# Kernel optimization log

Measured on AMD Instinct MI355X. Metric: run time of the kernel, lower is better.

## Reference

```python
import jax, jax.numpy as jnp
import numpy as np

N, E, H_DIM, HEADS = 20000, 640000, 128, 8
HD = H_DIM // HEADS  # head_dim = 16


def setup_inputs() -> dict:
    key = jax.random.key(0)
    ks = jax.random.split(key, 12)
    def xavier(k, shape):
        fan_in, fan_out = shape[0], shape[1]
        lim = jnp.sqrt(6.0 / (fan_in + fan_out))
        return jax.random.uniform(k, shape, jnp.float32, -lim, lim)
    return {
        "x": jax.random.normal(ks[0], (N, H_DIM), jnp.float32),
        "edge_index": jax.random.randint(ks[1], (2, E), 0, N, jnp.int64 if jax.config.x64_enabled else jnp.int32),
        "edge_attr": jax.random.normal(ks[2], (E, H_DIM), jnp.float32),
        "WQ": xavier(ks[3], (H_DIM, H_DIM)),
        "WK": xavier(ks[4], (H_DIM, H_DIM)),
        "WV": xavier(ks[5], (H_DIM, H_DIM)),
        "WE": xavier(ks[6], (H_DIM, H_DIM)),
        "Wout": xavier(ks[7], (H_DIM, H_DIM)),
        "bout": jnp.zeros((H_DIM,), jnp.float32),
        "gn_w": jnp.ones((H_DIM,), jnp.float32),
        "gn_b": jnp.zeros((H_DIM,), jnp.float32),
        "gn_ms": jnp.ones((H_DIM,), jnp.float32),
    }


def reference(x, edge_index, edge_attr, WQ, WK, WV, WE, Wout, bout, gn_w, gn_b, gn_ms):
    n = x.shape[0]
    src, dst = edge_index[0], edge_index[1]  # PyG: row=source j, col=target i

    q = (x @ WQ).reshape(n, HEADS, HD)
    k = (x @ WK).reshape(n, HEADS, HD)
    v = (x @ WV).reshape(n, HEADS, HD)
    e = (edge_attr @ WE).reshape(-1, HEADS, HD)

    # per-edge attention score [E, HEADS]
    score = jnp.sum(q[dst] * (k[src] + e), axis=-1) / jnp.sqrt(jnp.asarray(HD, x.dtype))

    # scatter-softmax over edges grouped by destination node
    seg_max = jax.ops.segment_max(score, dst, num_segments=n)  # [N, HEADS]
    seg_max = jnp.where(jnp.isfinite(seg_max), seg_max, 0.0)
    ex = jnp.exp(score - seg_max[dst])
    denom = jax.ops.segment_sum(ex, dst, num_segments=n)
    alpha = ex / (denom[dst] + 1e-16)  # [E, HEADS]

    # weighted scatter-add aggregation
    msg = alpha[..., None] * (v[src] + e)  # [E, HEADS, HD]
    out = jax.ops.segment_sum(msg, dst, num_segments=n).reshape(n, H_DIM)

    out = out @ Wout + bout
    h = out + x  # residual (DropPath is identity in eval)

    # GraphNorm with batch=None -> single-graph normalization
    mean = jnp.mean(h, axis=0)
    o = h - mean * gn_ms
    var = jnp.mean(o * o, axis=0)
    o = gn_w * o / jnp.sqrt(var + 1e-5) + gn_b

    return jax.nn.gelu(o, approximate=False)
```

## Files before the change

kernel.cpp:

```cpp
#include <hip/hip_runtime.h>

using u16 = unsigned short;
using u32 = unsigned int;
typedef float f32x4 __attribute__((ext_vector_type(4)));
typedef short s16x8 __attribute__((ext_vector_type(8)));
typedef u32   u32x2 __attribute__((ext_vector_type(2)));
typedef u32   u32x4 __attribute__((ext_vector_type(4)));

__device__ __forceinline__ u16 f2bf(float f) {
  u32 u = __float_as_uint(f);
  u += 0x7fffu + ((u >> 16) & 1u);
  return (u16)(u >> 16);
}
__device__ __forceinline__ float bf2f(u16 h) {
  return __uint_as_float(((u32)h) << 16);
}

__global__ void ROEN_Final_33526514713351_kernel() {}


__global__ void roen_zero(int* __restrict__ count, int N, float* __restrict__ dbg) {
  int i = blockIdx.x * 256 + threadIdx.x;
  if (i == 0) dbg[0] = 1000.0f;
  if (i < N) count[i] = 0;
}

__global__ void roen_hist(const int* __restrict__ ei, int E, int* __restrict__ count,
                          float* __restrict__ dbg) {
  int i = blockIdx.x * 256 + threadIdx.x;
  if (i == 0) dbg[1] = 1001.0f;
  if (i < E) atomicAdd(&count[ei[E + i]], 1);
}

__global__ __launch_bounds__(256) void roen_scan(const int* __restrict__ count, int N,
                                                 int* __restrict__ off, int* __restrict__ cursor,
                                                 float* __restrict__ dbg) {
  __shared__ int tsum[256];
  int tid = threadIdx.x;
  if (tid == 0) dbg[2] = 1002.0f;
  int chunk = (N + 255) / 256;
  int b = tid * chunk;
  int e = b + chunk; if (e > N) e = N; if (b > N) b = N;
  int s = 0;
  for (int i = b; i < e; ++i) s += count[i];
  tsum[tid] = s;
  __syncthreads();
  for (int d = 1; d < 256; d <<= 1) {
    int t = (tid >= d) ? tsum[tid - d] : 0;
    __syncthreads();
    tsum[tid] += t;
    __syncthreads();
  }
  int run = tsum[tid] - s;
  for (int i = b; i < e; ++i) {
    off[i] = run; cursor[i] = run;
    run += count[i];
  }
  if (tid == 255) off[N] = run;
}

__global__ void roen_scatter(const int* __restrict__ ei, int E, int* __restrict__ cursor,
                             int* __restrict__ inv, int* __restrict__ srcS,
                             int* __restrict__ dstS, float* __restrict__ dbg) {
  int i = blockIdx.x * 256 + threadIdx.x;
  if (i == 0) dbg[3] = 1003.0f;
  if (i < E) {
    int s = ei[i];
    int d = ei[E + i];
    int p = atomicAdd(&cursor[d], 1);
    inv[i] = p;
    srcS[p] = s;
    dstS[p] = d;
  }
}

__global__ void roen_prep_w(const float* __restrict__ W0, const float* __restrict__ W1,
                            const float* __restrict__ W2, const float* __restrict__ W3,
                            const float* __restrict__ W4, u16* __restrict__ Wt,
                            float* __restrict__ dbg) {
  int w = blockIdx.x;
  if (w == 0 && threadIdx.x == 0) dbg[4] = 1004.0f;
  const float* W = (w == 0) ? W0 : (w == 1) ? W1 : (w == 2) ? W2 : (w == 3) ? W3 : W4;
  for (int idx = threadIdx.x; idx < 16384; idx += 256) {
    int n = idx >> 7, k = idx & 127;
    Wt[w * 16384 + idx] = f2bf(W[k * 128 + n]);
  }
}

__global__ __launch_bounds__(256) void roen_gemm_qkv(const float* __restrict__ x,
                                                     const u16* __restrict__ Wt,
                                                     u16* __restrict__ qb, u16* __restrict__ kb,
                                                     u32* __restrict__ vb2, int M,
                                                     float* __restrict__ dbg) {
  __shared__ u16 As[64 * 128];
  const int tid = threadIdx.x;
  if (blockIdx.x == 0 && tid == 0) dbg[5] = 1005.0f;
  const long brow = (long)blockIdx.x * 64;

  {
    f32x4 tmp[8];
#pragma unroll
    for (int j = 0; j < 8; ++j) {
      int idx = j * 256 + tid;
      int row = idx >> 5;
      int c4 = (idx & 31) * 4;
      long grow = brow + row;
      f32x4 a = {0.f, 0.f, 0.f, 0.f};
      if (grow < M) a = *(const f32x4*)(x + grow * 128 + c4);
      tmp[j] = a;
    }
#pragma unroll
    for (int j = 0; j < 8; ++j) {
      int idx = j * 256 + tid;
      int row = idx >> 5;
      int c4 = (idx & 31) * 4;
      u32 lo = ((u32)f2bf(tmp[j][1]) << 16) | (u32)f2bf(tmp[j][0]);
      u32 hi = ((u32)f2bf(tmp[j][3]) << 16) | (u32)f2bf(tmp[j][2]);
      int byte = (row * 256 + c4 * 2) ^ ((row & 7) << 4);
      u32x2 val; val[0] = lo; val[1] = hi;
      *(u32x2*)((char*)As + byte) = val;
    }
  }
  __syncthreads();

  const int wave = tid >> 6, lane = tid & 63;
  const int wc = wave * 32;
  const int lr = lane & 15, lg = lane >> 4;

  s16x8 af[4][4];
#pragma unroll
  for (int ks = 0; ks < 4; ++ks) {
    int kb2 = (ks * 32 + lg * 8) * 2;
#pragma unroll
    for (int mt = 0; mt < 4; ++mt) {
      int row = mt * 16 + lr;
      int byte = (row * 256 + kb2) ^ ((row & 7) << 4);
      af[ks][mt] = *(const s16x8*)((const char*)As + byte);
    }
  }

  for (int w = 0; w < 3; ++w) {
    s16x8 bfr[4][2];
#pragma unroll
    for (int ks = 0; ks < 4; ++ks)
#pragma unroll
      for (int nt = 0; nt < 2; ++nt)
        bfr[ks][nt] = *(const s16x8*)(Wt + w * 16384 + (wc + nt * 16 + lr) * 128 + ks * 32 + lg * 8);

    f32x4 acc[4][2];
    for (int mt = 0; mt < 4; ++mt)
      for (int nt = 0; nt < 2; ++nt) acc[mt][nt] = {0.f, 0.f, 0.f, 0.f};

#pragma unroll
    for (int ks = 0; ks < 4; ++ks)
      for (int mt = 0; mt < 4; ++mt)
        for (int nt = 0; nt < 2; ++nt)
          acc[mt][nt] = __builtin_amdgcn_mfma_f32_16x16x32_bf16(af[ks][mt], bfr[ks][nt], acc[mt][nt], 0, 0, 0);

    if (w == 2) {
      for (int mt = 0; mt < 4; ++mt) {
        for (int r = 0; r < 4; ++r) {
          long row = brow + mt * 16 + lg * 4 + r;
          if (row < M) {
            u32 val = (u32)f2bf(acc[mt][0][r]) | ((u32)f2bf(acc[mt][1][r]) << 16);
            vb2[row * 64 + wave * 16 + lr] = val;
          }
        }
      }
    } else {
      u16* C = (w == 0) ? qb : kb;
      for (int mt = 0; mt < 4; ++mt) {
        for (int nt = 0; nt < 2; ++nt) {
          int col = wc + nt * 16 + lr;
          for (int r = 0; r < 4; ++r) {
            long row = brow + mt * 16 + lg * 4 + r;
            if (row < M) C[row * 128 + col] = f2bf(acc[mt][nt][r]);
          }
        }
      }
    }
  }
}

__global__ __launch_bounds__(256) void roen_gemm_e(const float* __restrict__ ea,
                                                   const u16* __restrict__ WtE,
                                                   const int* __restrict__ inv,
                                                   u32* __restrict__ eS2, int E,
                                                   float* __restrict__ dbg) {
  __shared__ u16 As[128 * 128];
  __shared__ int invv[128];
  const int tid = threadIdx.x;
  if (blockIdx.x == 0 && tid == 0) dbg[6] = 1006.0f;
  const long brow = (long)blockIdx.x * 128;

  if (tid < 128) {
    long pos = brow + tid;
    invv[tid] = (pos < E) ? inv[pos] : -1;
  }

  {
    f32x4 tmp[16];
#pragma unroll
    for (int j = 0; j < 16; ++j) {
      int idx = j * 256 + tid;
      int row = idx >> 5;
      int c4 = (idx & 31) * 4;
      long grow = brow + row;
      f32x4 a = {0.f, 0.f, 0.f, 0.f};
      if (grow < E) a = *(const f32x4*)(ea + grow * 128 + c4);
      tmp[j] = a;
    }
#pragma unroll
    for (int j = 0; j < 16; ++j) {
      int idx = j * 256 + tid;
      int row = idx >> 5;
      int c4 = (idx & 31) * 4;
      u32 lo = ((u32)f2bf(tmp[j][1]) << 16) | (u32)f2bf(tmp[j][0]);
      u32 hi = ((u32)f2bf(tmp[j][3]) << 16) | (u32)f2bf(tmp[j][2]);
      int byte = (row * 256 + c4 * 2) ^ ((row & 7) << 4);
      u32x2 val; val[0] = lo; val[1] = hi;
      *(u32x2*)((char*)As + byte) = val;
    }
  }

  const int wave = tid >> 6, lane = tid & 63;
  const int wc = wave * 32;
  const int lr = lane & 15, lg = lane >> 4;

  s16x8 bfr[4][2];
#pragma unroll
  for (int ks = 0; ks < 4; ++ks)
#pragma unroll
    for (int nt = 0; nt < 2; ++nt)
      bfr[ks][nt] = *(const s16x8*)(WtE + (wc + nt * 16 + lr) * 128 + ks * 32 + lg * 8);

  __syncthreads();

  f32x4 acc[8][2];
  for (int mt = 0; mt < 8; ++mt)
    for (int nt = 0; nt < 2; ++nt) acc[mt][nt] = {0.f, 0.f, 0.f, 0.f};

  for (int ks = 0; ks < 4; ++ks) {
    int kb2 = (ks * 32 + lg * 8) * 2;
    s16x8 af[8];
    for (int mt = 0; mt < 8; ++mt) {
      int row = mt * 16 + lr;
      int byte = (row * 256 + kb2) ^ ((row & 7) << 4);
      af[mt] = *(const s16x8*)((const char*)As + byte);
    }
    for (int mt = 0; mt < 8; ++mt)
      for (int nt = 0; nt < 2; ++nt)
        acc[mt][nt] = __builtin_amdgcn_mfma_f32_16x16x32_bf16(af[mt], bfr[ks][nt], acc[mt][nt], 0, 0, 0);
  }

  for (int mt = 0; mt < 8; ++mt) {
    for (int r = 0; r < 4; ++r) {
      int row = mt * 16 + lg * 4 + r;
      int op = invv[row];
      if (op >= 0) {
        u32 val = (u32)f2bf(acc[mt][0][r]) | ((u32)f2bf(acc[mt][1][r]) << 16);
        eS2[(long)op * 64 + wave * 16 + lr] = val;
      }
    }
  }
}

__global__ __launch_bounds__(256) void roen_score(const int* __restrict__ srcS,
                                                  const int* __restrict__ dstS,
                                                  const u16* __restrict__ qb,
                                                  const u16* __restrict__ kb,
                                                  const u32* __restrict__ eS2,
                                                  float* __restrict__ wS, int E,
                                                  float* __restrict__ dbg) {
  long gid = (long)blockIdx.x * 256 + threadIdx.x;
  if (gid == 0) dbg[9] = 1009.0f;
  long pos = gid >> 3;
  int h = (int)(gid & 7);
  if (pos >= E) return;
  int dst = dstS[pos], src = srcS[pos];
  const s16x8* qp = (const s16x8*)(qb + (long)dst * 128 + h * 16);
  const s16x8* kp = (const s16x8*)(kb + (long)src * 128 + h * 16);
  const u32x4* ep = (const u32x4*)(eS2 + (long)pos * 64 + (h >> 1) * 16);
  const int sh = (h & 1) * 16;
  float acc = 0.f;
#pragma unroll
  for (int c = 0; c < 2; ++c) {
    s16x8 qv = qp[c], kv = kp[c];
    u32x4 ea_ = ep[c * 2], eb_ = ep[c * 2 + 1];
#pragma unroll
    for (int j = 0; j < 4; ++j) {
      float e0 = bf2f((u16)(ea_[j] >> sh));
      float e1 = bf2f((u16)(eb_[j] >> sh));
      acc += bf2f((u16)qv[j]) * (bf2f((u16)kv[j]) + e0);
      acc += bf2f((u16)qv[j + 4]) * (bf2f((u16)kv[j + 4]) + e1);
    }
  }
  wS[pos * 8 + h] = __expf(fminf(acc * 0.25f, 80.f));
}

__global__ __launch_bounds__(256) void roen_node_agg(const int* __restrict__ off,
                                                     const int* __restrict__ srcS,
                                                     const u32* __restrict__ eS2,
                                                     const u32* __restrict__ vb2,
                                                     const float* __restrict__ wS,
                                                     float* __restrict__ outat, int N,
                                                     float* __restrict__ dbg) {
  int wave = threadIdx.x >> 6;
  int lane = threadIdx.x & 63;
  int node = blockIdx.x * 4 + wave;
  if (node == 0 && lane == 0) dbg[10] = 1010.0f;
  if (node >= N) return;
  int beg = off[node], end = off[node + 1];

  const int dA = 32 * (lane >> 4) + (lane & 15);
  const int dB = dA + 16;
  const int hA = dA >> 4;
  const int hB = hA + 1;
  float accA = 0.f, accB = 0.f, dsA = 0.f, dsB = 0.f;

  int pos = beg;
  for (; pos + 4 <= end; pos += 4) {
    int s0 = srcS[pos], s1 = srcS[pos + 1], s2 = srcS[pos + 2], s3 = srcS[pos + 3];
    float wa0 = wS[(long)(pos + 0) * 8 + hA], wb0 = wS[(long)(pos + 0) * 8 + hB];
    float wa1 = wS[(long)(pos + 1) * 8 + hA], wb1 = wS[(long)(pos + 1) * 8 + hB];
    float wa2 = wS[(long)(pos + 2) * 8 + hA], wb2 = wS[(long)(pos + 2) * 8 + hB];
    float wa3 = wS[(long)(pos + 3) * 8 + hA], wb3 = wS[(long)(pos + 3) * 8 + hB];
    u32 e0 = eS2[(long)(pos + 0) * 64 + lane];
    u32 e1 = eS2[(long)(pos + 1) * 64 + lane];
    u32 e2 = eS2[(long)(pos + 2) * 64 + lane];
    u32 e3 = eS2[(long)(pos + 3) * 64 + lane];
    u32 v0 = vb2[(long)s0 * 64 + lane];
    u32 v1 = vb2[(long)s1 * 64 + lane];
    u32 v2 = vb2[(long)s2 * 64 + lane];
    u32 v3 = vb2[(long)s3 * 64 + lane];
    accA += wa0 * (bf2f((u16)v0) + bf2f((u16)e0));
    accB += wb0 * (bf2f((u16)(v0 >> 16)) + bf2f((u16)(e0 >> 16)));
    accA += wa1 * (bf2f((u16)v1) + bf2f((u16)e1));
    accB += wb1 * (bf2f((u16)(v1 >> 16)) + bf2f((u16)(e1 >> 16)));
    accA += wa2 * (bf2f((u16)v2) + bf2f((u16)e2));
    accB += wb2 * (bf2f((u16)(v2 >> 16)) + bf2f((u16)(e2 >> 16)));
    accA += wa3 * (bf2f((u16)v3) + bf2f((u16)e3));
    accB += wb3 * (bf2f((u16)(v3 >> 16)) + bf2f((u16)(e3 >> 16)));
    dsA += wa0 + wa1 + wa2 + wa3;
    dsB += wb0 + wb1 + wb2 + wb3;
  }
  for (; pos < end; ++pos) {
    float wa = wS[(long)pos * 8 + hA], wb = wS[(long)pos * 8 + hB];
    u32 ev = eS2[(long)pos * 64 + lane];
    int src = srcS[pos];
    u32 vv = vb2[(long)src * 64 + lane];
    accA += wa * (bf2f((u16)vv) + bf2f((u16)ev));
    accB += wb * (bf2f((u16)(vv >> 16)) + bf2f((u16)(ev >> 16)));
    dsA += wa; dsB += wb;
  }
  outat[(long)node * 128 + dA] = accA / (dsA + 1e-16f);
  outat[(long)node * 128 + dB] = accB / (dsB + 1e-16f);
}

__global__ __launch_bounds__(256) void roen_gemm_out(const float* __restrict__ A,
                                                     const u16* __restrict__ Wt,
                                                     const float* __restrict__ x,
                                                     const float* __restrict__ bo,
                                                     float* __restrict__ h,
                                                     float* __restrict__ psum,
                                                     float* __restrict__ psumsq, int M,
                                                     float* __restrict__ dbg) {
  __shared__ u16 As[64 * 128];
  const int tid = threadIdx.x;
  if (blockIdx.x == 0 && tid == 0) dbg[11] = 1011.0f;
  const long brow = (long)blockIdx.x * 64;

  {
    f32x4 tmp[8];
#pragma unroll
    for (int j = 0; j < 8; ++j) {
      int idx = j * 256 + tid;
      int row = idx >> 5;
      int c4 = (idx & 31) * 4;
      long grow = brow + row;
      f32x4 a = {0.f, 0.f, 0.f, 0.f};
      if (grow < M) a = *(const f32x4*)(A + grow * 128 + c4);
      tmp[j] = a;
    }
#pragma unroll
    for (int j = 0; j < 8; ++j) {
      int idx = j * 256 + tid;
      int row = idx >> 5;
      int c4 = (idx & 31) * 4;
      u32 lo = ((u32)f2bf(tmp[j][1]) << 16) | (u32)f2bf(tmp[j][0]);
      u32 hi = ((u32)f2bf(tmp[j][3]) << 16) | (u32)f2bf(tmp[j][2]);
      int byte = (row * 256 + c4 * 2) ^ ((row & 7) << 4);
      u32x2 val; val[0] = lo; val[1] = hi;
      *(u32x2*)((char*)As + byte) = val;
    }
  }

  const int wave = tid >> 6, lane = tid & 63;
  const int wc = wave * 32;
  const int lr = lane & 15, lg = lane >> 4;

  s16x8 bfr[4][2];
#pragma unroll
  for (int ks = 0; ks < 4; ++ks)
#pragma unroll
    for (int nt = 0; nt < 2; ++nt)
      bfr[ks][nt] = *(const s16x8*)(Wt + (wc + nt * 16 + lr) * 128 + ks * 32 + lg * 8);

  __syncthreads();

  f32x4 acc[4][2];
  for (int mt = 0; mt < 4; ++mt)
    for (int nt = 0; nt < 2; ++nt) acc[mt][nt] = {0.f, 0.f, 0.f, 0.f};

  for (int ks = 0; ks < 4; ++ks) {
    int kb2 = (ks * 32 + lg * 8) * 2;
    s16x8 af[4];
    for (int mt = 0; mt < 4; ++mt) {
      int row = mt * 16 + lr;
      int byte = (row * 256 + kb2) ^ ((row & 7) << 4);
      af[mt] = *(const s16x8*)((const char*)As + byte);
    }
    for (int mt = 0; mt < 4; ++mt)
      for (int nt = 0; nt < 2; ++nt)
        acc[mt][nt] = __builtin_amdgcn_mfma_f32_16x16x32_bf16(af[mt], bfr[ks][nt], acc[mt][nt], 0, 0, 0);
  }

  float b0 = bo[wc + lr];
  float b1 = bo[wc + 16 + lr];
  float cs[2] = {0.f, 0.f}, cs2[2] = {0.f, 0.f};
  for (int mt = 0; mt < 4; ++mt) {
    for (int nt = 0; nt < 2; ++nt) {
      int col = wc + nt * 16 + lr;
      float bb = (nt == 0) ? b0 : b1;
      for (int r = 0; r < 4; ++r) {
        long row = brow + mt * 16 + lg * 4 + r;
        if (row < M) {
          long idx = row * 128 + col;
          float val = acc[mt][nt][r] + bb + x[idx];
          h[idx] = val;
          cs[nt] += val;
          cs2[nt] += val * val;
        }
      }
    }
  }
#pragma unroll
  for (int nt = 0; nt < 2; ++nt) {
    cs[nt] += __shfl_xor(cs[nt], 16);
    cs[nt] += __shfl_xor(cs[nt], 32);
    cs2[nt] += __shfl_xor(cs2[nt], 16);
    cs2[nt] += __shfl_xor(cs2[nt], 32);
  }
  if (lg == 0) {
    int col0 = wc + lr;
    psum[(long)blockIdx.x * 128 + col0] = cs[0];
    psumsq[(long)blockIdx.x * 128 + col0] = cs2[0];
    psum[(long)blockIdx.x * 128 + col0 + 16] = cs[1];
    psumsq[(long)blockIdx.x * 128 + col0 + 16] = cs2[1];
  }
}

__global__ void roen_stats(const float* __restrict__ psum, const float* __restrict__ psumsq,
                           const float* __restrict__ gnw, const float* __restrict__ gnb,
                           const float* __restrict__ gnms, float* __restrict__ Ac,
                           float* __restrict__ Bc, int nb, int N, float* __restrict__ dbg) {
  int d = threadIdx.x;
  if (d == 0) dbg[13] = 1013.0f;
  float s = 0.f, s2 = 0.f;
  for (int i = 0; i < nb; ++i) {
    s += psum[(long)i * 128 + d];
    s2 += psumsq[(long)i * 128 + d];
  }
  float mean = s / (float)N;
  float mm = mean * gnms[d];
  float var = s2 / (float)N - 2.f * mm * mean + mm * mm;
  float scale = gnw[d] * rsqrtf(var + 1e-5f);
  Ac[d] = scale;
  Bc[d] = gnb[d] - mm * scale;
}

__global__ __launch_bounds__(256) void roen_final(const float* __restrict__ h,
                                                  const float* __restrict__ Ac,
                                                  const float* __restrict__ Bc,
                                                  float* __restrict__ out, long total) {
  long i = (long)blockIdx.x * 256 + threadIdx.x;
  if (i >= total) return;
  int d = (int)(i & 127);
  float v = h[i] * Ac[d] + Bc[d];
  out[i] = 0.5f * v * (1.f + erff(v * 0.70710678f));
}

extern "C" void kernel_launch(void* const* d_in, const int* in_sizes, int n_in,
                              void* d_out, int out_size, void* d_ws, size_t ws_size,
                              hipStream_t stream) {
  const float* x   = (const float*)d_in[0];
  const int*   ei  = (const int*)d_in[1];
  const float* ea  = (const float*)d_in[2];
  const float* WQ  = (const float*)d_in[3];
  const float* WK  = (const float*)d_in[4];
  const float* WV  = (const float*)d_in[5];
  const float* WE  = (const float*)d_in[6];
  const float* Wo  = (const float*)d_in[7];
  const float* bo  = (const float*)d_in[8];
  const float* gnw = (const float*)d_in[9];
  const float* gnb = (const float*)d_in[10];
  const float* gnms= (const float*)d_in[11];
  float* out = (float*)d_out;
  float* dbg = (float*)d_out;

  const int N = in_sizes[0] / 128;
  const int E = in_sizes[1] / 2;
  const int gN = (N + 63) / 64;

  char* base = (char*)d_ws;
  size_t cur = 0;
  auto alloc = [&](size_t bytes) -> char* {
    char* r = base + cur;
    cur = (cur + bytes + 255) & ~(size_t)255;
    return r;
  };
  u16*   wt     = (u16*)alloc(5 * 16384 * sizeof(u16));
  u16*   qb     = (u16*)alloc((size_t)N * 128 * sizeof(u16));
  u16*   kb     = (u16*)alloc((size_t)N * 128 * sizeof(u16));
  u32*   vb2    = (u32*)alloc((size_t)N * 64 * sizeof(u32));
  float* wS     = (float*)alloc((size_t)E * 8 * sizeof(float));
  int*   count  = (int*)alloc((size_t)N * sizeof(int));
  int*   offar  = (int*)alloc((size_t)(N + 1) * sizeof(int));
  int*   cursor = (int*)alloc((size_t)N * sizeof(int));
  int*   invar  = (int*)alloc((size_t)E * sizeof(int));
  int*   srcS   = (int*)alloc((size_t)E * sizeof(int));
  int*   dstS   = (int*)alloc((size_t)E * sizeof(int));
  float* outat  = (float*)alloc((size_t)N * 128 * sizeof(float));
  float* psum   = (float*)alloc((size_t)gN * 128 * sizeof(float));
  float* psumsq = (float*)alloc((size_t)gN * 128 * sizeof(float));
  float* Ac     = (float*)alloc(128 * sizeof(float));
  float* Bc     = (float*)alloc(128 * sizeof(float));
  u32*   eS2    = (u32*)alloc((size_t)E * 64 * sizeof(u32));
  float* hbuf   = (float*)eS2;

  roen_zero<<<(N + 255) / 256, 256, 0, stream>>>(count, N, dbg);
  roen_hist<<<(E + 255) / 256, 256, 0, stream>>>(ei, E, count, dbg);
  roen_scan<<<1, 256, 0, stream>>>(count, N, offar, cursor, dbg);
  roen_scatter<<<(E + 255) / 256, 256, 0, stream>>>(ei, E, cursor, invar, srcS, dstS, dbg);
  roen_prep_w<<<5, 256, 0, stream>>>(WQ, WK, WV, WE, Wo, wt, dbg);

  roen_gemm_qkv<<<gN, 256, 0, stream>>>(x, wt, qb, kb, vb2, N, dbg);
  roen_gemm_e<<<(E + 127) / 128, 256, 0, stream>>>(ea, wt + 3 * 16384, invar, eS2, E, dbg);

  roen_score<<<(int)(((long)E * 8 + 255) / 256), 256, 0, stream>>>(srcS, dstS, qb, kb, eS2, wS, E, dbg);
  roen_node_agg<<<(N + 3) / 4, 256, 0, stream>>>(offar, srcS, eS2, vb2, wS, outat, N, dbg);

  roen_gemm_out<<<gN, 256, 0, stream>>>(outat, wt + 4 * 16384, x, bo, hbuf, psum, psumsq, N, dbg);
  roen_stats<<<1, 128, 0, stream>>>(psum, psumsq, gnw, gnb, gnms, Ac, Bc, gN, N, dbg);
  roen_final<<<(int)(((long)N * 128 + 255) / 256), 256, 0, stream>>>(hbuf, Ac, Bc, out, (long)N * 128);
}
```

Baseline: 457.6 us.

## Capture atomic ranks for CSR build, parallelize scan, shrink edge GEMM tiles

The histogram kernel now records each edge's atomic rank, so the scatter computes its position as off[d]+rank and no longer needs a second atomic pass over a cursor array. The single-block scan becomes a 1024-thread wave-shuffle scan in place of a 256-thread serial chunked scan. The edge GEMM tile drops from 128 to 64 rows per block, which halves LDS use so more blocks fit per CU. The node aggregation loads its two head weights with one 2-float vector load. The CSR order within each node now follows the histogram atomics, and an extra E-sized rank array is written and read.

Measured after the change: 415.3 us. -9.2%, faster.

```diff
diff --git a/kernel.cpp b/kernel.cpp
--- a/kernel.cpp
+++ b/kernel.cpp
@@ -3,6 +3,7 @@
 using u16 = unsigned short;
 using u32 = unsigned int;
 typedef float f32x4 __attribute__((ext_vector_type(4)));
+typedef float f32x2 __attribute__((ext_vector_type(2)));
 typedef short s16x8 __attribute__((ext_vector_type(8)));
 typedef u32   u32x2 __attribute__((ext_vector_type(2)));
 typedef u32   u32x4 __attribute__((ext_vector_type(4)));
@@ -26,50 +27,62 @@
 }
 
 __global__ void roen_hist(const int* __restrict__ ei, int E, int* __restrict__ count,
-                          float* __restrict__ dbg) {
+                          int* __restrict__ rank, float* __restrict__ dbg) {
   int i = blockIdx.x * 256 + threadIdx.x;
   if (i == 0) dbg[1] = 1001.0f;
-  if (i < E) atomicAdd(&count[ei[E + i]], 1);
-}
-
-__global__ __launch_bounds__(256) void roen_scan(const int* __restrict__ count, int N,
-                                                 int* __restrict__ off, int* __restrict__ cursor,
-                                                 float* __restrict__ dbg) {
-  __shared__ int tsum[256];
-  int tid = threadIdx.x;
-  if (tid == 0) dbg[2] = 1002.0f;
-  int chunk = (N + 255) / 256;
-  int b = tid * chunk;
-  int e = b + chunk; if (e > N) e = N; if (b > N) b = N;
-  int s = 0;
-  for (int i = b; i < e; ++i) s += count[i];
-  tsum[tid] = s;
+  if (i < E) rank[i] = atomicAdd(&count[ei[E + i]], 1);
+}
+
+__global__ __launch_bounds__(1024) void roen_scan(const int* __restrict__ count, int N,
+                                                  int* __restrict__ off,
+                                                  float* __restrict__ dbg) {
+  __shared__ int wsum[16];
+  __shared__ int carrys;
+  int tid = threadIdx.x, lane = tid & 63, wv = tid >> 6;
+  if (tid == 0) { dbg[2] = 1002.0f; carrys = 0; }
   __syncthreads();
-  for (int d = 1; d < 256; d <<= 1) {
-    int t = (tid >= d) ? tsum[tid - d] : 0;
+  for (int base = 0; base < N; base += 1024) {
+    int i = base + tid;
+    int v = (i < N) ? count[i] : 0;
+    int x = v;
+#pragma unroll
+    for (int s = 1; s < 64; s <<= 1) {
+      int t = __shfl_up(x, s);
+      if (lane >= s) x += t;
+    }
+    if (lane == 63) wsum[wv] = x;
     __syncthreads();
-    tsum[tid] += t;
+    if (wv == 0 && lane < 16) {
+      int y = wsum[lane];
+#pragma unroll
+      for (int s = 1; s < 16; s <<= 1) {
+        int t = __shfl_up(y, s);
+        if (lane >= s) y += t;
+      }
+      wsum[lane] = y;
+    }
     __syncthreads();
-  }
-  int run = tsum[tid] - s;
-  for (int i = b; i < e; ++i) {
-    off[i] = run; cursor[i] = run;
-    run += count[i];
-  }
-  if (tid == 255) off[N] = run;
-}
-
-__global__ void roen_scatter(const int* __restrict__ ei, int E, int* __restrict__ cursor,
+    int wbase = (wv == 0) ? 0 : wsum[wv - 1];
+    int incl = x + wbase + carrys;
+    if (i < N) off[i] = incl - v;
+    __syncthreads();
+    if (tid == 1023) carrys = incl;
+    __syncthreads();
+  }
+  if (tid == 0) off[N] = carrys;
+}
+
+__global__ void roen_scatter(const int* __restrict__ ei, const int* __restrict__ off,
+                             const int* __restrict__ rank, int E,
                              int* __restrict__ inv, int* __restrict__ srcS,
                              int* __restrict__ dstS, float* __restrict__ dbg) {
   int i = blockIdx.x * 256 + threadIdx.x;
   if (i == 0) dbg[3] = 1003.0f;
   if (i < E) {
-    int s = ei[i];
     int d = ei[E + i];
-    int p = atomicAdd(&cursor[d], 1);
+    int p = off[d] + rank[i];
     inv[i] = p;
-    srcS[p] = s;
+    srcS[p] = ei[i];
     dstS[p] = d;
   }
 }
@@ -187,21 +200,21 @@
                                                    const int* __restrict__ inv,
                                                    u32* __restrict__ eS2, int E,
                                                    float* __restrict__ dbg) {
-  __shared__ u16 As[128 * 128];
-  __shared__ int invv[128];
+  __shared__ u16 As[64 * 128];
+  __shared__ int invv[64];
   const int tid = threadIdx.x;
   if (blockIdx.x == 0 && tid == 0) dbg[6] = 1006.0f;
-  const long brow = (long)blockIdx.x * 128;
-
-  if (tid < 128) {
+  const long brow = (long)blockIdx.x * 64;
+
+  if (tid < 64) {
     long pos = brow + tid;
     invv[tid] = (pos < E) ? inv[pos] : -1;
   }
 
   {
-    f32x4 tmp[16];
-#pragma unroll
-    for (int j = 0; j < 16; ++j) {
+    f32x4 tmp[8];
+#pragma unroll
+    for (int j = 0; j < 8; ++j) {
       int idx = j * 256 + tid;
       int row = idx >> 5;
       int c4 = (idx & 31) * 4;
@@ -211,7 +224,7 @@
       tmp[j] = a;
     }
 #pragma unroll
-    for (int j = 0; j < 16; ++j) {
+    for (int j = 0; j < 8; ++j) {
       int idx = j * 256 + tid;
       int row = idx >> 5;
       int c4 = (idx & 31) * 4;
@@ -222,6 +235,7 @@
       *(u32x2*)((char*)As + byte) = val;
     }
   }
+  __syncthreads();
 
   const int wave = tid >> 6, lane = tid & 63;
   const int wc = wave * 32;
@@ -234,26 +248,24 @@
     for (int nt = 0; nt < 2; ++nt)
       bfr[ks][nt] = *(const s16x8*)(WtE + (wc + nt * 16 + lr) * 128 + ks * 32 + lg * 8);
 
-  __syncthreads();
-
-  f32x4 acc[8][2];
-  for (int mt = 0; mt < 8; ++mt)
+  f32x4 acc[4][2];
+  for (int mt = 0; mt < 4; ++mt)
     for (int nt = 0; nt < 2; ++nt) acc[mt][nt] = {0.f, 0.f, 0.f, 0.f};
 
   for (int ks = 0; ks < 4; ++ks) {
     int kb2 = (ks * 32 + lg * 8) * 2;
-    s16x8 af[8];
-    for (int mt = 0; mt < 8; ++mt) {
+    s16x8 af[4];
+    for (int mt = 0; mt < 4; ++mt) {
       int row = mt * 16 + lr;
       int byte = (row * 256 + kb2) ^ ((row & 7) << 4);
       af[mt] = *(const s16x8*)((const char*)As + byte);
     }
-    for (int mt = 0; mt < 8; ++mt)
+    for (int mt = 0; mt < 4; ++mt)
       for (int nt = 0; nt < 2; ++nt)
         acc[mt][nt] = __builtin_amdgcn_mfma_f32_16x16x32_bf16(af[mt], bfr[ks][nt], acc[mt][nt], 0, 0, 0);
   }
 
-  for (int mt = 0; mt < 8; ++mt) {
+  for (int mt = 0; mt < 4; ++mt) {
     for (int r = 0; r < 4; ++r) {
       int row = mt * 16 + lg * 4 + r;
       int op = invv[row];
@@ -315,16 +327,15 @@
   const int dA = 32 * (lane >> 4) + (lane & 15);
   const int dB = dA + 16;
   const int hA = dA >> 4;
-  const int hB = hA + 1;
   float accA = 0.f, accB = 0.f, dsA = 0.f, dsB = 0.f;
 
   int pos = beg;
   for (; pos + 4 <= end; pos += 4) {
     int s0 = srcS[pos], s1 = srcS[pos + 1], s2 = srcS[pos + 2], s3 = srcS[pos + 3];
-    float wa0 = wS[(long)(pos + 0) * 8 + hA], wb0 = wS[(long)(pos + 0) * 8 + hB];
-    float wa1 = wS[(long)(pos + 1) * 8 + hA], wb1 = wS[(long)(pos + 1) * 8 + hB];
-    float wa2 = wS[(long)(pos + 2) * 8 + hA], wb2 = wS[(long)(pos + 2) * 8 + hB];
-    float wa3 = wS[(long)(pos + 3) * 8 + hA], wb3 = wS[(long)(pos + 3) * 8 + hB];
+    f32x2 w0 = *(const f32x2*)(wS + (long)(pos + 0) * 8 + hA);
+    f32x2 w1 = *(const f32x2*)(wS + (long)(pos + 1) * 8 + hA);
+    f32x2 w2 = *(const f32x2*)(wS + (long)(pos + 2) * 8 + hA);
+    f32x2 w3 = *(const f32x2*)(wS + (long)(pos + 3) * 8 + hA);
     u32 e0 = eS2[(long)(pos + 0) * 64 + lane];
     u32 e1 = eS2[(long)(pos + 1) * 64 + lane];
     u32 e2 = eS2[(long)(pos + 2) * 64 + lane];
@@ -333,25 +344,25 @@
     u32 v1 = vb2[(long)s1 * 64 + lane];
     u32 v2 = vb2[(long)s2 * 64 + lane];
     u32 v3 = vb2[(long)s3 * 64 + lane];
-    accA += wa0 * (bf2f((u16)v0) + bf2f((u16)e0));
-    accB += wb0 * (bf2f((u16)(v0 >> 16)) + bf2f((u16)(e0 >> 16)));
-    accA += wa1 * (bf2f((u16)v1) + bf2f((u16)e1));
-    accB += wb1 * (bf2f((u16)(v1 >> 16)) + bf2f((u16)(e1 >> 16)));
-    accA += wa2 * (bf2f((u16)v2) + bf2f((u16)e2));
-    accB += wb2 * (bf2f((u16)(v2 >> 16)) + bf2f((u16)(e2 >> 16)));
-    accA += wa3 * (bf2f((u16)v3) + bf2f((u16)e3));
-    accB += wb3 * (bf2f((u16)(v3 >> 16)) + bf2f((u16)(e3 >> 16)));
-    dsA += wa0 + wa1 + wa2 + wa3;
-    dsB += wb0 + wb1 + wb2 + wb3;
+    accA += w0[0] * (bf2f((u16)v0) + bf2f((u16)e0));
+    accB += w0[1] * (bf2f((u16)(v0 >> 16)) + bf2f((u16)(e0 >> 16)));
+    accA += w1[0] * (bf2f((u16)v1) + bf2f((u16)e1));
+    accB += w1[1] * (bf2f((u16)(v1 >> 16)) + bf2f((u16)(e1 >> 16)));
+    accA += w2[0] * (bf2f((u16)v2) + bf2f((u16)e2));
+    accB += w2[1] * (bf2f((u16)(v2 >> 16)) + bf2f((u16)(e2 >> 16)));
+    accA += w3[0] * (bf2f((u16)v3) + bf2f((u16)e3));
+    accB += w3[1] * (bf2f((u16)(v3 >> 16)) + bf2f((u16)(e3 >> 16)));
+    dsA += w0[0] + w1[0] + w2[0] + w3[0];
+    dsB += w0[1] + w1[1] + w2[1] + w3[1];
   }
   for (; pos < end; ++pos) {
-    float wa = wS[(long)pos * 8 + hA], wb = wS[(long)pos * 8 + hB];
+    f32x2 w = *(const f32x2*)(wS + (long)pos * 8 + hA);
     u32 ev = eS2[(long)pos * 64 + lane];
     int src = srcS[pos];
     u32 vv = vb2[(long)src * 64 + lane];
-    accA += wa * (bf2f((u16)vv) + bf2f((u16)ev));
-    accB += wb * (bf2f((u16)(vv >> 16)) + bf2f((u16)(ev >> 16)));
-    dsA += wa; dsB += wb;
+    accA += w[0] * (bf2f((u16)vv) + bf2f((u16)ev));
+    accB += w[1] * (bf2f((u16)(vv >> 16)) + bf2f((u16)(ev >> 16)));
+    dsA += w[0]; dsB += w[1];
   }
   outat[(long)node * 128 + dA] = accA / (dsA + 1e-16f);
   outat[(long)node * 128 + dB] = accB / (dsB + 1e-16f);
@@ -526,7 +537,7 @@
   float* wS     = (float*)alloc((size_t)E * 8 * sizeof(float));
   int*   count  = (int*)alloc((size_t)N * sizeof(int));
   int*   offar  = (int*)alloc((size_t)(N + 1) * sizeof(int));
-  int*   cursor = (int*)alloc((size_t)N * sizeof(int));
+  int*   rank   = (int*)alloc((size_t)E * sizeof(int));
   int*   invar  = (int*)alloc((size_t)E * sizeof(int));
   int*   srcS   = (int*)alloc((size_t)E * sizeof(int));
   int*   dstS   = (int*)alloc((size_t)E * sizeof(int));
@@ -539,13 +550,13 @@
   float* hbuf   = (float*)eS2;
 
   roen_zero<<<(N + 255) / 256, 256, 0, stream>>>(count, N, dbg);
-  roen_hist<<<(E + 255) / 256, 256, 0, stream>>>(ei, E, count, dbg);
-  roen_scan<<<1, 256, 0, stream>>>(count, N, offar, cursor, dbg);
-  roen_scatter<<<(E + 255) / 256, 256, 0, stream>>>(ei, E, cursor, invar, srcS, dstS, dbg);
+  roen_hist<<<(E + 255) / 256, 256, 0, stream>>>(ei, E, count, rank, dbg);
+  roen_scan<<<1, 1024, 0, stream>>>(count, N, offar, dbg);
+  roen_scatter<<<(E + 255) / 256, 256, 0, stream>>>(ei, offar, rank, E, invar, srcS, dstS, dbg);
   roen_prep_w<<<5, 256, 0, stream>>>(WQ, WK, WV, WE, Wo, wt, dbg);
 
   roen_gemm_qkv<<<gN, 256, 0, stream>>>(x, wt, qb, kb, vb2, N, dbg);
-  roen_gemm_e<<<(E + 127) / 128, 256, 0, stream>>>(ea, wt + 3 * 16384, invar, eS2, E, dbg);
+  roen_gemm_e<<<(E + 63) / 64, 256, 0, stream>>>(ea, wt + 3 * 16384, invar, eS2, E, dbg);
 
   roen_score<<<(int)(((long)E * 8 + 255) / 256), 256, 0, stream>>>(srcS, dstS, qb, kb, eS2, wS, E, dbg);
   roen_node_agg<<<(N + 3) / 4, 256, 0, stream>>>(offar, srcS, eS2, vb2, wS, outat, N, dbg);
```
